# Performance work log

Hardware: AMD Instinct MI355X
Metric: run time of the kernel (lower is better)

The kernel has to match this reference:

```python
import jax, jax.numpy as jnp
import numpy as np

N_WIRES = 8
N_QLAYERS = 1
DIM = 1 << N_WIRES  # 256

# bits[s, w] = w-th bit of basis state s; wire 0 is the MOST significant bit
# (torchquantum stores states as [bsz, 2, 2, ..., 2] with wire i at axis i+1)
_BITS = ((np.arange(DIM)[:, None] >> (N_WIRES - 1 - np.arange(N_WIRES))) & 1).astype(np.float32)


def setup_inputs() -> dict:
    key = jax.random.key(0)
    ks = jax.random.split(key, 5)
    pi = float(np.pi)
    return {
        "input_features": jax.random.normal(ks[0], (4, 4096, N_WIRES), jnp.float32),
        "params_ry1": jax.random.uniform(ks[1], (N_QLAYERS, N_WIRES), jnp.float32, -pi, pi),
        "params_crz1": jax.random.uniform(ks[2], (N_QLAYERS, N_WIRES), jnp.float32, -pi, pi),
        "params_ry2": jax.random.uniform(ks[3], (N_QLAYERS, N_WIRES), jnp.float32, -pi, pi),
        "params_crz2": jax.random.uniform(ks[4], (N_QLAYERS, N_WIRES), jnp.float32, -pi, pi),
    }


def _apply_ry(state, wire, theta):
    """Apply RY(theta) = [[c,-s],[s,c]] (c=cos(theta/2)) on `wire`.
    theta: scalar (shared param) or [B] (batched encoder angle)."""
    B = state.shape[0]
    c = jnp.cos(theta * 0.5)
    s = jnp.sin(theta * 0.5)
    if jnp.ndim(theta):  # per-batch angle
        c = c[:, None, None]
        s = s[:, None, None]
    st = state.reshape(B, 1 << wire, 2, -1)
    a, b = st[:, :, 0, :], st[:, :, 1, :]
    return jnp.stack([c * a - s * b, s * a + c * b], axis=2).reshape(B, DIM)


def _crz_block_diag(controls, targets, thetas, bits):
    """Fused diagonal of a commuting block of CRZ gates.
    CRZ(c,t,th) = diag over basis: 1 if bit_c==0 else exp(+/- i th/2) for bit_t=1/0.
    exponent contribution: bit_c * th * (bit_t - 0.5)."""
    expo = (bits[:, controls] * (bits[:, targets] - 0.5)) @ thetas  # [DIM]
    return jnp.exp(1j * expo).astype(jnp.complex64)


def _vqc_forward(x, params_ry1, params_crz1, params_ry2, params_crz2):
    B = x.shape[0]
    bits = jnp.asarray(_BITS)
    # |0...0>
    state = jnp.zeros((B, DIM), jnp.complex64).at[:, 0].set(1.0)

    idx = np.arange(N_WIRES)
    ctrl1, tgt1 = idx, (idx + 1) % N_WIRES  # crz block 1: wires [i, i+1]
    ctrl2, tgt2 = idx, (idx - 1) % N_WIRES  # crz block 2: wires [i, i-1]

    for k in range(N_QLAYERS):
        # tensor-product encoder: RY(x_i) on wire i
        for i in range(N_WIRES):
            state = _apply_ry(state, i, x[:, i])
        # CRZ ring (all diagonal -> fused)
        state = state * _crz_block_diag(ctrl1, tgt1, params_crz1[k], bits)[None, :]
        # trainable RY layer 1
        for i in range(N_WIRES):
            state = _apply_ry(state, i, params_ry1[k, i])
        # reverse CRZ ring (diagonal -> fused)
        state = state * _crz_block_diag(ctrl2, tgt2, params_crz2[k], bits)[None, :]
        # trainable RY layer 2
        for i in range(N_WIRES):
            state = _apply_ry(state, i, params_ry2[k, i])

    # PauliZ expectation on every wire: <Z_w> = sum_s |amp_s|^2 * (1 - 2*bit_w(s))
    probs = (state.real ** 2 + state.imag ** 2)  # [B, DIM]
    signs = 1.0 - 2.0 * bits                      # [DIM, N_WIRES]
    return probs @ signs                          # [B, N_WIRES]


def reference(input_features, params_ry1, params_crz1, params_ry2, params_crz2):
    bsz, slen, fz = input_features.shape
    x = input_features.reshape(-1, fz)
    out = _vqc_forward(x, params_ry1, params_crz1, params_ry2, params_crz2)
    return out.reshape(bsz, slen, fz)
```

## Files before the change

### kernel.cpp

```cpp
#include <hip/hip_runtime.h>
#include <math.h>

#define NW 8
#define DIM 256

__global__ __launch_bounds__(256) void vqc_kernel(
    const float* __restrict__ x,
    const float* __restrict__ ry1,
    const float* __restrict__ crz1,
    const float* __restrict__ ry2,
    const float* __restrict__ crz2,
    float* __restrict__ out,
    int B)
{
    __shared__ float4 pc1[DIM / 4], ps1[DIM / 4], pc2[DIM / 4], ps2[DIM / 4];

    const int t = threadIdx.x;
    {
        float e1 = 0.f, e2 = 0.f;
#pragma unroll
        for (int i = 0; i < NW; ++i) {
            float bc  = (float)((t >> (7 - i)) & 1);
            float bt1 = (float)((t >> (7 - ((i + 1) & 7))) & 1);
            float bt2 = (float)((t >> (7 - ((i + 7) & 7))) & 1);
            e1 += bc * crz1[i] * (bt1 - 0.5f);
            e2 += bc * crz2[i] * (bt2 - 0.5f);
        }
        float s, c;
        __sincosf(e1, &s, &c);
        ((float*)pc1)[t] = c; ((float*)ps1)[t] = s;
        __sincosf(e2, &s, &c);
        ((float*)pc2)[t] = c; ((float*)ps2)[t] = s;
    }
    __syncthreads();

    const int lane = t & 63;

    float rc1[8], rs1[8], rc2[8], rs2[8];
#pragma unroll
    for (int i = 0; i < 8; ++i) {
        __sincosf(0.5f * ry1[i], &rs1[i], &rc1[i]);
        __sincosf(0.5f * ry2[i], &rs2[i], &rc2[i]);
    }

    const float4 c1 = pc1[lane], s1 = ps1[lane];
    const float4 c2 = pc2[lane], s2 = ps2[lane];

    const int wavesPerBlock = blockDim.x >> 6;
    int gw = blockIdx.x * wavesPerBlock + (t >> 6);
    const int TW = gridDim.x * wavesPerBlock;

#define RY_LAYER(RC, RS)                                                    \
    do {                                                                    \
        _Pragma("unroll")                                                   \
        for (int i = 0; i < 6; ++i) {                                       \
            float c = RC[i], s = RS[i];                                     \
            const int mask = 1 << (5 - i);                                  \
            float se = (lane & mask) ? s : -s;                              \
            _Pragma("unroll")                                               \
            for (int j = 0; j < 4; ++j) {                                   \
                float pre = __shfl_xor(re[j], mask);                        \
                float pim = __shfl_xor(im[j], mask);                        \
                re[j] = fmaf(se, pre, c * re[j]);                           \
                im[j] = fmaf(se, pim, c * im[j]);                           \
            }                                                               \
        }                                                                   \
        {                       \
            float c = RC[6], s = RS[6];                                     \
            float nr0 = c * re[0] - s * re[2], nr2 = fmaf(s, re[0], c * re[2]); \
            float nr1 = c * re[1] - s * re[3], nr3 = fmaf(s, re[1], c * re[3]); \
            float ni0 = c * im[0] - s * im[2], ni2 = fmaf(s, im[0], c * im[2]); \
            float ni1 = c * im[1] - s * im[3], ni3 = fmaf(s, im[1], c * im[3]); \
            re[0] = nr0; re[1] = nr1; re[2] = nr2; re[3] = nr3;             \
            im[0] = ni0; im[1] = ni1; im[2] = ni2; im[3] = ni3;             \
        }                                                                   \
        {                       \
            float c = RC[7], s = RS[7];                                     \
            float nr0 = c * re[0] - s * re[1], nr1 = fmaf(s, re[0], c * re[1]); \
            float nr2 = c * re[2] - s * re[3], nr3 = fmaf(s, re[2], c * re[3]); \
            float ni0 = c * im[0] - s * im[1], ni1 = fmaf(s, im[0], c * im[1]); \
            float ni2 = c * im[2] - s * im[3], ni3 = fmaf(s, im[2], c * im[3]); \
            re[0] = nr0; re[1] = nr1; re[2] = nr2; re[3] = nr3;             \
            im[0] = ni0; im[1] = ni1; im[2] = ni2; im[3] = ni3;             \
        }                                                                   \
    } while (0)

    for (int b = gw; b < B; b += TW) {
        const float4* xp = (const float4*)(x + (size_t)b * NW);
        float4 xa = xp[0], xb = xp[1];
        float cs[8], sn[8];
        __sincosf(0.5f * xa.x, &sn[0], &cs[0]);
        __sincosf(0.5f * xa.y, &sn[1], &cs[1]);
        __sincosf(0.5f * xa.z, &sn[2], &cs[2]);
        __sincosf(0.5f * xa.w, &sn[3], &cs[3]);
        __sincosf(0.5f * xb.x, &sn[4], &cs[4]);
        __sincosf(0.5f * xb.y, &sn[5], &cs[5]);
        __sincosf(0.5f * xb.z, &sn[6], &cs[6]);
        __sincosf(0.5f * xb.w, &sn[7], &cs[7]);

        float pr = 1.f;
        pr *= (lane & 32) ? sn[0] : cs[0];
        pr *= (lane & 16) ? sn[1] : cs[1];
        pr *= (lane & 8)  ? sn[2] : cs[2];
        pr *= (lane & 4)  ? sn[3] : cs[3];
        pr *= (lane & 2)  ? sn[4] : cs[4];
        pr *= (lane & 1)  ? sn[5] : cs[5];
        float a0 = pr * cs[6] * cs[7];
        float a1 = pr * cs[6] * sn[7];
        float a2 = pr * sn[6] * cs[7];
        float a3 = pr * sn[6] * sn[7];

        float re[4], im[4];
        re[0] = a0 * c1.x; im[0] = a0 * s1.x;
        re[1] = a1 * c1.y; im[1] = a1 * s1.y;
        re[2] = a2 * c1.z; im[2] = a2 * s1.z;
        re[3] = a3 * c1.w; im[3] = a3 * s1.w;

        RY_LAYER(rc1, rs1);

        {
            float nr, ni;
            nr = re[0] * c2.x - im[0] * s2.x; ni = re[0] * s2.x + im[0] * c2.x; re[0] = nr; im[0] = ni;
            nr = re[1] * c2.y - im[1] * s2.y; ni = re[1] * s2.y + im[1] * c2.y; re[1] = nr; im[1] = ni;
            nr = re[2] * c2.z - im[2] * s2.z; ni = re[2] * s2.z + im[2] * c2.z; re[2] = nr; im[2] = ni;
            nr = re[3] * c2.w - im[3] * s2.w; ni = re[3] * s2.w + im[3] * c2.w; re[3] = nr; im[3] = ni;
        }

        RY_LAYER(rc2, rs2);

        float p0 = re[0] * re[0] + im[0] * im[0];
        float p1 = re[1] * re[1] + im[1] * im[1];
        float p2 = re[2] * re[2] + im[2] * im[2];
        float p3 = re[3] * re[3] + im[3] * im[3];

        float v0 = (p0 + p1) + (p2 + p3);
        float v6 = (p0 + p1) - (p2 + p3);
        float v7 = (p0 - p1) + (p2 - p3);

#pragma unroll
        for (int m = 1; m <= 32; m <<= 1) {
            float o0 = __shfl_xor(v0, m);
            float o6 = __shfl_xor(v6, m);
            float o7 = __shfl_xor(v7, m);
            if (lane & m) { v0 = o0 - v0; v6 = o6 - v6; v7 = o7 - v7; }
            else          { v0 = o0 + v0; v6 = o6 + v6; v7 = o7 + v7; }
        }

        float* ob = out + (size_t)b * NW;
        if (lane == 0) {
            ob[6] = v6;
            ob[7] = v7;
        } else {
            int k = __ffs(lane) - 1;
            if (lane == (1 << k) && k <= 5)
                ob[5 - k] = v0;
        }
    }
#undef RY_LAYER
}

extern "C" void kernel_launch(void* const* d_in, const int* in_sizes, int n_in,
                              void* d_out, int out_size, void* d_ws, size_t ws_size,
                              hipStream_t stream) {
    const float* x    = (const float*)d_in[0];
    const float* ry1  = (const float*)d_in[1];
    const float* crz1 = (const float*)d_in[2];
    const float* ry2  = (const float*)d_in[3];
    const float* crz2 = (const float*)d_in[4];
    float* out = (float*)d_out;

    int B = in_sizes[0] / NW;
    int blocks = (B + 3) / 4;
    if (blocks < 1) blocks = 1;
    vqc_kernel<<<blocks, 256, 0, stream>>>(x, ry1, crz1, ry2, crz2, out, B);
}
```

Before: 82.01 us.

## Pack four samples per wavefront with 16 amplitudes per lane and DPP exchanges

```diff
diff --git a/kernel.cpp b/kernel.cpp
--- a/kernel.cpp
+++ b/kernel.cpp
@@ -2,7 +2,19 @@
 #include <math.h>
 
 #define NW 8
-#define DIM 256
+
+template<int CTRL>
+__device__ __forceinline__ float dpp_x(float v) {
+    return __int_as_float(
+        __builtin_amdgcn_update_dpp(0, __float_as_int(v), CTRL, 0xF, 0xF, true));
+}
+__device__ __forceinline__ float swz_xor4(float v) {
+    return __int_as_float(__builtin_amdgcn_ds_swizzle(__float_as_int(v), 0x101F));
+}
+#define XCH1(v) dpp_x<0xB1>(v)
+#define XCH2(v) dpp_x<0x4E>(v)
+#define XCH8(v) dpp_x<0x128>(v)
+#define XCH4(v) swz_xor4(v)
 
 __global__ __launch_bounds__(256) void vqc_kernel(
     const float* __restrict__ x,
@@ -13,28 +25,34 @@
     float* __restrict__ out,
     int B)
 {
-    __shared__ float4 pc1[DIM / 4], ps1[DIM / 4], pc2[DIM / 4], ps2[DIM / 4];
+    __shared__ __align__(16) float Tc1[320], Ts1[320], Tc2[320], Ts2[320];
 
     const int t = threadIdx.x;
     {
+        const int n = t;
         float e1 = 0.f, e2 = 0.f;
 #pragma unroll
         for (int i = 0; i < NW; ++i) {
-            float bc  = (float)((t >> (7 - i)) & 1);
-            float bt1 = (float)((t >> (7 - ((i + 1) & 7))) & 1);
-            float bt2 = (float)((t >> (7 - ((i + 7) & 7))) & 1);
+            float bc  = (float)((n >> (7 - i)) & 1);
+            float bt1 = (float)((n >> (7 - ((i + 1) & 7))) & 1);
+            float bt2 = (float)((n >> (7 - ((i + 7) & 7))) & 1);
             e1 += bc * crz1[i] * (bt1 - 0.5f);
             e2 += bc * crz2[i] * (bt2 - 0.5f);
         }
+        const int j  = n & 15;
+        const int nh = n >> 4;
+        const int sl = ((nh >> 3) & 1) | (((nh >> 2) & 1) << 1)
+                     | ((nh & 1) << 2) | (((nh >> 1) & 1) << 3);
+        const int idx = sl * 20 + j;
         float s, c;
-        __sincosf(e1, &s, &c);
-        ((float*)pc1)[t] = c; ((float*)ps1)[t] = s;
-        __sincosf(e2, &s, &c);
-        ((float*)pc2)[t] = c; ((float*)ps2)[t] = s;
+        __sincosf(e1, &s, &c);  Tc1[idx] = c;  Ts1[idx] = s;
+        __sincosf(e2, &s, &c);  Tc2[idx] = c;  Ts2[idx] = s;
     }
     __syncthreads();
 
     const int lane = t & 63;
+    const int sl   = lane & 15;
+    const int g    = lane >> 4;
 
     float rc1[8], rs1[8], rc2[8], rs2[8];
 #pragma unroll
@@ -43,50 +61,53 @@
         __sincosf(0.5f * ry2[i], &rs2[i], &rc2[i]);
     }
 
-    const float4 c1 = pc1[lane], s1 = ps1[lane];
-    const float4 c2 = pc2[lane], s2 = ps2[lane];
+    const float* pc1 = &Tc1[sl * 20];
+    const float* ps1 = &Ts1[sl * 20];
+    const float* pc2 = &Tc2[sl * 20];
+    const float* ps2 = &Ts2[sl * 20];
 
     const int wavesPerBlock = blockDim.x >> 6;
-    int gw = blockIdx.x * wavesPerBlock + (t >> 6);
+    const int gwave = blockIdx.x * wavesPerBlock + (t >> 6);
     const int TW = gridDim.x * wavesPerBlock;
+
+#define CROSS_WIRE(RC, RS, WI, SLBIT, EXCH)                                 \
+    { float c = RC[WI], s = RS[WI];                                         \
+      float se = (sl & SLBIT) ? s : -s;                                     \
+      _Pragma("unroll")                                                     \
+      for (int j = 0; j < 16; ++j) {                                        \
+          float pre = EXCH(re[j]);                                          \
+          float pim = EXCH(im[j]);                                          \
+          re[j] = fmaf(se, pre, c * re[j]);                                 \
+          im[j] = fmaf(se, pim, c * im[j]);                                 \
+      } }
+
+#define INLANE_WIRE(RC, RS, WI, M)                                          \
+    { float c = RC[WI], s = RS[WI];                                         \
+      _Pragma("unroll")                                                     \
+      for (int j = 0; j < 16; ++j) if (!(j & M)) {                          \
+          int hi = j | M;                                                   \
+          float rl = re[j], rh = re[hi], il = im[j], ih = im[hi];           \
+          re[j]  = c * rl - s * rh;  re[hi] = fmaf(s, rl, c * rh);          \
+          im[j]  = c * il - s * ih;  im[hi] = fmaf(s, il, c * ih);          \
+      } }
 
 #define RY_LAYER(RC, RS)                                                    \
     do {                                                                    \
-        _Pragma("unroll")                                                   \
-        for (int i = 0; i < 6; ++i) {                                       \
-            float c = RC[i], s = RS[i];                                     \
-            const int mask = 1 << (5 - i);                                  \
-            float se = (lane & mask) ? s : -s;                              \
-            _Pragma("unroll")                                               \
-            for (int j = 0; j < 4; ++j) {                                   \
-                float pre = __shfl_xor(re[j], mask);                        \
-                float pim = __shfl_xor(im[j], mask);                        \
-                re[j] = fmaf(se, pre, c * re[j]);                           \
-                im[j] = fmaf(se, pim, c * im[j]);                           \
-            }                                                               \
-        }                                                                   \
-        {                       \
-            float c = RC[6], s = RS[6];                                     \
-            float nr0 = c * re[0] - s * re[2], nr2 = fmaf(s, re[0], c * re[2]); \
-            float nr1 = c * re[1] - s * re[3], nr3 = fmaf(s, re[1], c * re[3]); \
-            float ni0 = c * im[0] - s * im[2], ni2 = fmaf(s, im[0], c * im[2]); \
-            float ni1 = c * im[1] - s * im[3], ni3 = fmaf(s, im[1], c * im[3]); \
-            re[0] = nr0; re[1] = nr1; re[2] = nr2; re[3] = nr3;             \
-            im[0] = ni0; im[1] = ni1; im[2] = ni2; im[3] = ni3;             \
-        }                                                                   \
-        {                       \
-            float c = RC[7], s = RS[7];                                     \
-            float nr0 = c * re[0] - s * re[1], nr1 = fmaf(s, re[0], c * re[1]); \
-            float nr2 = c * re[2] - s * re[3], nr3 = fmaf(s, re[2], c * re[3]); \
-            float ni0 = c * im[0] - s * im[1], ni1 = fmaf(s, im[0], c * im[1]); \
-            float ni2 = c * im[2] - s * im[3], ni3 = fmaf(s, im[2], c * im[3]); \
-            re[0] = nr0; re[1] = nr1; re[2] = nr2; re[3] = nr3;             \
-            im[0] = ni0; im[1] = ni1; im[2] = ni2; im[3] = ni3;             \
-        }                                                                   \
+        CROSS_WIRE(RC, RS, 0, 1, XCH1);                                     \
+        CROSS_WIRE(RC, RS, 1, 2, XCH2);                                     \
+        CROSS_WIRE(RC, RS, 2, 8, XCH8);                                     \
+        CROSS_WIRE(RC, RS, 3, 4, XCH4);                                     \
+        INLANE_WIRE(RC, RS, 4, 8);                                          \
+        INLANE_WIRE(RC, RS, 5, 4);                                          \
+        INLANE_WIRE(RC, RS, 6, 2);                                          \
+        INLANE_WIRE(RC, RS, 7, 1);                                          \
     } while (0)
 
-    for (int b = gw; b < B; b += TW) {
-        const float4* xp = (const float4*)(x + (size_t)b * NW);
+    for (int b0 = gwave * 4; b0 < B; b0 += TW * 4) {
+        const int b  = b0 + g;
+        const int bl = (b < B) ? b : (B - 1);
+
+        const float4* xp = (const float4*)(x + (size_t)bl * NW);
         float4 xa = xp[0], xb = xp[1];
         float cs[8], sn[8];
         __sincosf(0.5f * xa.x, &sn[0], &cs[0]);
@@ -98,65 +119,87 @@
         __sincosf(0.5f * xb.z, &sn[6], &cs[6]);
         __sincosf(0.5f * xb.w, &sn[7], &cs[7]);
 
-        float pr = 1.f;
-        pr *= (lane & 32) ? sn[0] : cs[0];
-        pr *= (lane & 16) ? sn[1] : cs[1];
-        pr *= (lane & 8)  ? sn[2] : cs[2];
-        pr *= (lane & 4)  ? sn[3] : cs[3];
-        pr *= (lane & 2)  ? sn[4] : cs[4];
-        pr *= (lane & 1)  ? sn[5] : cs[5];
-        float a0 = pr * cs[6] * cs[7];
-        float a1 = pr * cs[6] * sn[7];
-        float a2 = pr * sn[6] * cs[7];
-        float a3 = pr * sn[6] * sn[7];
-
-        float re[4], im[4];
-        re[0] = a0 * c1.x; im[0] = a0 * s1.x;
-        re[1] = a1 * c1.y; im[1] = a1 * s1.y;
-        re[2] = a2 * c1.z; im[2] = a2 * s1.z;
-        re[3] = a3 * c1.w; im[3] = a3 * s1.w;
+        float pcf = ((sl & 1) ? sn[0] : cs[0])
+                  * ((sl & 2) ? sn[1] : cs[1])
+                  * ((sl & 8) ? sn[2] : cs[2])
+                  * ((sl & 4) ? sn[3] : cs[3]);
+
+        float a[16];
+#pragma unroll
+        for (int j = 0; j < 16; ++j) {
+            float f = ((j & 1) ? sn[7] : cs[7]);
+            f *= ((j & 2) ? sn[6] : cs[6]);
+            f *= ((j & 4) ? sn[5] : cs[5]);
+            f *= ((j & 8) ? sn[4] : cs[4]);
+            a[j] = pcf * f;
+        }
+
+        float re[16], im[16];
+#pragma unroll
+        for (int q = 0; q < 4; ++q) {
+            float4 cq = *(const float4*)&pc1[4 * q];
+            float4 sq = *(const float4*)&ps1[4 * q];
+            re[4*q+0] = a[4*q+0] * cq.x;  im[4*q+0] = a[4*q+0] * sq.x;
+            re[4*q+1] = a[4*q+1] * cq.y;  im[4*q+1] = a[4*q+1] * sq.y;
+            re[4*q+2] = a[4*q+2] * cq.z;  im[4*q+2] = a[4*q+2] * sq.z;
+            re[4*q+3] = a[4*q+3] * cq.w;  im[4*q+3] = a[4*q+3] * sq.w;
+        }
 
         RY_LAYER(rc1, rs1);
 
-        {
+#pragma unroll
+        for (int q = 0; q < 4; ++q) {
+            float4 cq = *(const float4*)&pc2[4 * q];
+            float4 sq = *(const float4*)&ps2[4 * q];
             float nr, ni;
-            nr = re[0] * c2.x - im[0] * s2.x; ni = re[0] * s2.x + im[0] * c2.x; re[0] = nr; im[0] = ni;
-            nr = re[1] * c2.y - im[1] * s2.y; ni = re[1] * s2.y + im[1] * c2.y; re[1] = nr; im[1] = ni;
-            nr = re[2] * c2.z - im[2] * s2.z; ni = re[2] * s2.z + im[2] * c2.z; re[2] = nr; im[2] = ni;
-            nr = re[3] * c2.w - im[3] * s2.w; ni = re[3] * s2.w + im[3] * c2.w; re[3] = nr; im[3] = ni;
+            nr = re[4*q+0]*cq.x - im[4*q+0]*sq.x; ni = re[4*q+0]*sq.x + im[4*q+0]*cq.x; re[4*q+0] = nr; im[4*q+0] = ni;
+            nr = re[4*q+1]*cq.y - im[4*q+1]*sq.y; ni = re[4*q+1]*sq.y + im[4*q+1]*cq.y; re[4*q+1] = nr; im[4*q+1] = ni;
+            nr = re[4*q+2]*cq.z - im[4*q+2]*sq.z; ni = re[4*q+2]*sq.z + im[4*q+2]*cq.z; re[4*q+2] = nr; im[4*q+2] = ni;
+            nr = re[4*q+3]*cq.w - im[4*q+3]*sq.w; ni = re[4*q+3]*sq.w + im[4*q+3]*cq.w; re[4*q+3] = nr; im[4*q+3] = ni;
         }
 
         RY_LAYER(rc2, rs2);
 
-        float p0 = re[0] * re[0] + im[0] * im[0];
-        float p1 = re[1] * re[1] + im[1] * im[1];
-        float p2 = re[2] * re[2] + im[2] * im[2];
-        float p3 = re[3] * re[3] + im[3] * im[3];
-
-        float v0 = (p0 + p1) + (p2 + p3);
-        float v6 = (p0 + p1) - (p2 + p3);
-        float v7 = (p0 - p1) + (p2 - p3);
-
-#pragma unroll
-        for (int m = 1; m <= 32; m <<= 1) {
-            float o0 = __shfl_xor(v0, m);
-            float o6 = __shfl_xor(v6, m);
-            float o7 = __shfl_xor(v7, m);
-            if (lane & m) { v0 = o0 - v0; v6 = o6 - v6; v7 = o7 - v7; }
-            else          { v0 = o0 + v0; v6 = o6 + v6; v7 = o7 + v7; }
-        }
-
-        float* ob = out + (size_t)b * NW;
-        if (lane == 0) {
-            ob[6] = v6;
-            ob[7] = v7;
-        } else {
-            int k = __ffs(lane) - 1;
-            if (lane == (1 << k) && k <= 5)
-                ob[5 - k] = v0;
+        float p[16];
+#pragma unroll
+        for (int j = 0; j < 16; ++j) p[j] = re[j]*re[j] + im[j]*im[j];
+
+        float s2_[8], v7 = 0.f;
+#pragma unroll
+        for (int k = 0; k < 8; ++k) { s2_[k] = p[2*k] + p[2*k+1]; v7 += p[2*k] - p[2*k+1]; }
+        float s4_[4], v6 = 0.f;
+#pragma unroll
+        for (int k = 0; k < 4; ++k) { s4_[k] = s2_[2*k] + s2_[2*k+1]; v6 += s2_[2*k] - s2_[2*k+1]; }
+        float s8a = s4_[0] + s4_[1], s8b = s4_[2] + s4_[3];
+        float v5 = (s4_[0] - s4_[1]) + (s4_[2] - s4_[3]);
+        float v4 = s8a - s8b;
+        float v0 = s8a + s8b;
+
+#define BFLY_R(EXCH, M)                                                     \
+        { float o0 = EXCH(v0), o4 = EXCH(v4), o5 = EXCH(v5),                \
+                o6 = EXCH(v6), o7 = EXCH(v7);                               \
+          if (sl & M) { v0 = o0 - v0; v4 = o4 - v4; v5 = o5 - v5;           \
+                        v6 = o6 - v6; v7 = o7 - v7; }                       \
+          else        { v0 = o0 + v0; v4 = o4 + v4; v5 = o5 + v5;           \
+                        v6 = o6 + v6; v7 = o7 + v7; } }
+        BFLY_R(XCH1, 1);
+        BFLY_R(XCH2, 2);
+        BFLY_R(XCH4, 4);
+        BFLY_R(XCH8, 8);
+#undef BFLY_R
+
+        if (b < B) {
+            float* ob = out + (size_t)b * NW;
+            if      (sl == 1) ob[0] = v0;
+            else if (sl == 2) ob[1] = v0;
+            else if (sl == 8) ob[2] = v0;
+            else if (sl == 4) ob[3] = v0;
+            else if (sl == 0) *(float4*)(ob + 4) = make_float4(v4, v5, v6, v7);
         }
     }
 #undef RY_LAYER
+#undef CROSS_WIRE
+#undef INLANE_WIRE
 }
 
 extern "C" void kernel_launch(void* const* d_in, const int* in_sizes, int n_in,
@@ -170,7 +213,7 @@
     float* out = (float*)d_out;
 
     int B = in_sizes[0] / NW;
-    int blocks = (B + 3) / 4;
+    int blocks = (B + 15) / 16;
     if (blocks < 1) blocks = 1;
     vqc_kernel<<<blocks, 256, 0, stream>>>(x, ry1, crz1, ry2, crz2, out, B);
 }
```

Measured after the change: 71.38 us. 1.15x faster.
